# Performance work log

Hardware: AMD Instinct MI355X
Metric: run time of the kernel (lower is better)

## Reference

```python
import jax, jax.numpy as jnp
import numpy as np

DIM, ATT, G, T, KL, B = 1024, 128, 8, 4096, 256, 8
GD = DIM // G
SCALE = 1.0 / np.sqrt(ATT)

def setup_inputs() -> dict:
    key = jax.random.key(0)
    ks = jax.random.split(key, 7)
    x = jax.random.normal(ks[0], (B, T, DIM), dtype=jnp.float32)
    # stacked per-group weights (einsum orientation: in_dim x out_dim)
    Wq = jax.random.normal(ks[1], (G, GD, ATT), dtype=jnp.float32) * (1.0 / np.sqrt(GD))
    Wk = jax.random.normal(ks[2], (G, GD, ATT), dtype=jnp.float32) * (1.0 / np.sqrt(GD))
    Wv = jax.random.normal(ks[3], (G, GD, GD), dtype=jnp.float32) * (1.0 / np.sqrt(GD))
    Wo = jax.random.normal(ks[4], (G, GD, GD), dtype=jnp.float32) * (1.0 / np.sqrt(GD))
    Pk = jax.random.normal(ks[5], (G, T, KL), dtype=jnp.float32) * (1.0 / np.sqrt(T))
    Pv = jax.random.normal(ks[6], (G, T, KL), dtype=jnp.float32) * (1.0 / np.sqrt(T))
    return {"x": x, "Wq": Wq, "Wk": Wk, "Wv": Wv, "Wo": Wo, "Pk": Pk, "Pv": Pv}

def reference(x, Wq, Wk, Wv, Wo, Pk, Pv):
    Bx, Tx, _ = x.shape
    xg = x.reshape(Bx, Tx, G, GD).transpose(0, 2, 1, 3)        # [B,G,T,gd]
    q = jnp.einsum('bgtd,gda->bgta', xg, Wq)                   # [B,G,T,att]
    k = jnp.einsum('bgtd,gda->bgta', xg, Wk)
    v = jnp.einsum('bgtd,gde->bgte', xg, Wv)                   # [B,G,T,gd]
    k_red = jnp.einsum('bgta,gtk->bgka', k, Pk)                # [B,G,kl,att]
    v_red = jnp.einsum('bgte,gtk->bgke', v, Pv)                # [B,G,kl,gd]
    att = jax.nn.softmax(jnp.einsum('bgta,bgka->bgtk', q, k_red) * SCALE, axis=-1)
    out = jnp.einsum('bgtk,bgke->bgte', att, v_red)            # [B,G,T,gd]
    out = jnp.einsum('bgte,gef->bgtf', out, Wo)                # per-group output proj
    return out.transpose(0, 2, 1, 3).reshape(Bx, Tx, DIM)      # concat groups on last dim
```

## Files before the change

### kernel.cpp

```cpp
#include <hip/hip_runtime.h>
#include <hip/hip_bf16.h>

#define NB 8
#define NG 8
#define NT 4096
#define NDIM 1024
#define NGD 128
#define NATT 128
#define NKL 256
#define FSCALE 0.08838834764831845f

typedef __bf16 bf16x8 __attribute__((ext_vector_type(8)));
typedef float f32x4 __attribute__((ext_vector_type(4)));
typedef ushort u16x8 __attribute__((ext_vector_type(8)));
typedef ushort u16x4 __attribute__((ext_vector_type(4)));

#define MFMA(a, b, c) __builtin_amdgcn_mfma_f32_16x16x32_bf16(a, b, c, 0, 0, 0)

__device__ __forceinline__ ushort f2bf(float f) {
  union { float f; unsigned u; } v; v.f = f;
  unsigned r = v.u + 0x7FFFu + ((v.u >> 16) & 1u);
  return (ushort)(r >> 16);
}

__device__ __forceinline__ void gload16(const ushort* g, ushort* l) {
  __builtin_amdgcn_global_load_lds(
      (const __attribute__((address_space(1))) unsigned int*)g,
      (__attribute__((address_space(3))) unsigned int*)l, 16, 0, 0);
}

__global__ __launch_bounds__(512) void k0_weights(
    const float* __restrict__ Wq, const float* __restrict__ Wk,
    const float* __restrict__ Wv, const float* __restrict__ Wo,
    ushort* __restrict__ WkQT, ushort* __restrict__ WvoT) {
  const int sel = blockIdx.x;
  const int g = blockIdx.y;
  __shared__ float A2[128 * 136];
  __shared__ float B2[128 * 136];
  const int tid = threadIdx.x;

  if (sel == 0) {
#pragma unroll
    for (int u = 0; u < 8; ++u) {
      const int c = tid + 512 * u;
      const int row = c >> 5, c4 = (c & 31) * 4;
      *(float4*)&A2[row * 136 + c4] =
          *(const float4*)&Wo[(size_t)g * 16384 + row * 128 + c4];
      const float4 v = *(const float4*)&Wv[(size_t)g * 16384 + row * 128 + c4];
      B2[(c4 + 0) * 136 + row] = v.x;
      B2[(c4 + 1) * 136 + row] = v.y;
      B2[(c4 + 2) * 136 + row] = v.z;
      B2[(c4 + 3) * 136 + row] = v.w;
    }
  } else {
#pragma unroll
    for (int u = 0; u < 8; ++u) {
      const int c = tid + 512 * u;
      const int row = c >> 5, c4 = (c & 31) * 4;
      const float4 q = *(const float4*)&Wq[(size_t)g * 16384 + row * 128 + c4];
      A2[(c4 + 0) * 136 + row] = q.x;
      A2[(c4 + 1) * 136 + row] = q.y;
      A2[(c4 + 2) * 136 + row] = q.z;
      A2[(c4 + 3) * 136 + row] = q.w;
      const float4 k = *(const float4*)&Wk[(size_t)g * 16384 + row * 128 + c4];
      B2[(c4 + 0) * 136 + row] = k.x;
      B2[(c4 + 1) * 136 + row] = k.y;
      B2[(c4 + 2) * 136 + row] = k.z;
      B2[(c4 + 3) * 136 + row] = k.w;
    }
  }
  __syncthreads();

  const int mr = tid >> 4;
  const int mc = tid & 15;
  float acc[4][8];
#pragma unroll
  for (int i = 0; i < 4; ++i)
#pragma unroll
    for (int j = 0; j < 8; ++j) acc[i][j] = 0.f;

#pragma unroll 4
  for (int k = 0; k < 128; ++k) {
    const float4 a = *(const float4*)&A2[k * 136 + mr * 4];
    const float4 b0 = *(const float4*)&B2[k * 136 + mc * 8];
    const float4 b1 = *(const float4*)&B2[k * 136 + mc * 8 + 4];
    const float av[4] = {a.x, a.y, a.z, a.w};
    const float bv[8] = {b0.x, b0.y, b0.z, b0.w, b1.x, b1.y, b1.z, b1.w};
#pragma unroll
    for (int i = 0; i < 4; ++i)
#pragma unroll
      for (int j = 0; j < 8; ++j) acc[i][j] += av[i] * bv[j];
  }

  const float sc = sel ? FSCALE : 1.f;
  ushort* dst = (sel ? WkQT : WvoT) + (size_t)g * 16384;
#pragma unroll
  for (int i = 0; i < 4; ++i) {
    u16x8 pk;
#pragma unroll
    for (int j = 0; j < 8; ++j) pk[j] = f2bf(acc[i][j] * sc);
    *(u16x8*)&dst[(size_t)(mr * 4 + i) * 128 + mc * 8] = pk;
  }
}

__global__ __launch_bounds__(256) void kt_xp(
    const float* __restrict__ x, const float* __restrict__ Pk,
    const float* __restrict__ Pv, ushort* __restrict__ xT,
    ushort* __restrict__ PkT, ushort* __restrict__ PvT) {
  __shared__ float buf[64 * 132];
  const int bid = blockIdx.x;
  const int tid = threadIdx.x;

  if (bid < 4096) {
    const int t0 = (bid & 63) * 64;
    const int bg = bid >> 6;
    const int b = bg >> 3, g = bg & 7;
#pragma unroll
    for (int u = 0; u < 8; ++u) {
      const int c = tid + 256 * u;
      const int row = c >> 5, c4 = (c & 31) * 4;
      *(float4*)&buf[row * 132 + c4] =
          *(const float4*)&x[((size_t)b * NT + t0 + row) * NDIM + g * 128 + c4];
    }
    __syncthreads();
    const int seg = tid & 7;
    const int d0 = tid >> 3;
#pragma unroll
    for (int u = 0; u < 4; ++u) {
      const int d = d0 + u * 32;
      u16x8 pk;
#pragma unroll
      for (int z = 0; z < 8; ++z) pk[z] = f2bf(buf[(seg * 8 + z) * 132 + d]);
      *(u16x8*)&xT[((size_t)bg * 128 + d) * NT + t0 + seg * 8] = pk;
    }
  } else {
    const int idx = bid - 4096;
    const float* P = (idx >> 10) ? Pv : Pk;
    ushort* PT = (idx >> 10) ? PvT : PkT;
    const int r_ = idx & 1023;
    const int t0 = (r_ & 63) * 64;
    const int klh = (r_ >> 6) & 1;
    const int g = (r_ >> 7) & 7;
#pragma unroll
    for (int u = 0; u < 8; ++u) {
      const int c = tid + 256 * u;
      const int row = c >> 5, c4 = (c & 31) * 4;
      *(float4*)&buf[row * 132 + c4] =
          *(const float4*)&P[((size_t)g * NT + t0 + row) * NKL + klh * 128 + c4];
    }
    __syncthreads();
    const int seg = tid & 7;
    const int k0_ = tid >> 3;
#pragma unroll
    for (int u = 0; u < 4; ++u) {
      const int kl = k0_ + u * 32;
      u16x8 pk;
#pragma unroll
      for (int z = 0; z < 8; ++z) pk[z] = f2bf(buf[(seg * 8 + z) * 132 + kl]);
      *(u16x8*)&PT[((size_t)g * NKL + klh * 128 + kl) * NT + t0 + seg * 8] = pk;
    }
  }
}

__global__ __launch_bounds__(256, 2) void k1_mfma(
    const ushort* __restrict__ PkT, const ushort* __restrict__ PvT,
    const ushort* __restrict__ xT, const ushort* __restrict__ WkQT,
    const ushort* __restrict__ WvoT, ushort* __restrict__ MQ,
    ushort* __restrict__ vo_redT) {
  const int bid = blockIdx.x;
  const int work = (bid & 7) * 32 + (bid >> 3);
  const int bg = work >> 2;
  const int sel = (work >> 1) & 1;
  const int klt = work & 1;
  const int g = bg & 7;
  const ushort* PT = (sel ? PvT : PkT) + ((size_t)g * NKL + klt * 128) * NT;
  const ushort* Xb = xT + (size_t)bg * 128 * NT;

  __shared__ ushort lds[32768];

  const int tid = threadIdx.x;
  const int w = tid >> 6, lane = tid & 63;
  const int l15 = lane & 15, l4 = lane >> 4;
  const int rh = (w & 1) * 64;
  const int ch = (w >> 1) * 64;
  const int srow = lane >> 3, sc = lane & 7;

  f32x4 acc[4][4];
  const f32x4 fz = {0.f, 0.f, 0.f, 0.f};
#pragma unroll
  for (int i = 0; i < 4; ++i)
#pragma unroll
    for (int j = 0; j < 4; ++j) acc[i][j] = fz;

#define K1_STAGE(buf, s)                                                      \
  {                                                                           \
    const int t0_ = (s) * 64;                                                 \
    ushort* Ab_ = &lds[(buf) * 16384];                                        \
    ushort* Bb_ = &lds[(buf) * 16384 + 8192];                                 \
    _Pragma("unroll") for (int u = 0; u < 4; ++u) {                           \
      const int row_ = w * 32 + u * 8 + srow;                                 \
      const size_t off_ = (size_t)row_ * NT + t0_ + ((sc ^ (row_ & 7)) << 3); \
      gload16(PT + off_, Ab_ + (w * 32 + u * 8) * 64);                        \
      gload16(Xb + off_, Bb_ + (w * 32 + u * 8) * 64);                        \
    }                                                                         \
  }

#define K1_COMPUTE(buf)                                                       \
  {                                                                           \
    const ushort* Ab_ = &lds[(buf) * 16384];                                  \
    const ushort* Bb_ = &lds[(buf) * 16384 + 8192];                           \
    _Pragma("unroll") for (int h = 0; h < 2; ++h) {                           \
      bf16x8 af_[4], bf_[4];                                                  \
      _Pragma("unroll") for (int i = 0; i < 4; ++i) {                         \
        const int row_ = rh + i * 16 + l15;                                   \
        af_[i] = *(const bf16x8*)&Ab_[row_ * 64 +                             \
                                      (((h * 4 + l4) ^ (row_ & 7)) << 3)];    \
      }                                                                       \
      _Pragma("unroll") for (int j = 0; j < 4; ++j) {                         \
        const int row_ = ch + j * 16 + l15;                                   \
        bf_[j] = *(const bf16x8*)&Bb_[row_ * 64 +                             \
                                      (((h * 4 + l4) ^ (row_ & 7)) << 3)];    \
      }                                                                       \
      _Pragma("unroll") for (int i = 0; i < 4; ++i)                           \
        _Pragma("unroll") for (int j = 0; j < 4; ++j)                         \
          acc[i][j] = MFMA(af_[i], bf_[j], acc[i][j]);                        \
    }                                                                         \
  }

  K1_STAGE(0, 0);
  __syncthreads();
  int buf = 0;
#pragma unroll 1
  for (int s = 0; s < 64; ++s) {
    if (s + 1 < 64) K1_STAGE(buf ^ 1, s + 1);
    K1_COMPUTE(buf);
    __syncthreads();
    buf ^= 1;
  }

  ushort* C = lds;
#pragma unroll
  for (int i = 0; i < 4; ++i)
#pragma unroll
    for (int j = 0; j < 4; ++j)
#pragma unroll
      for (int r = 0; r < 4; ++r)
        C[(rh + i * 16 + l4 * 4 + r) * 136 + ch + j * 16 + l15] =
            f2bf(acc[i][j][r]);
  __syncthreads();

  const ushort* WT = (sel ? WvoT : WkQT) + (size_t)g * 16384;
  f32x4 o[4][4];
#pragma unroll
  for (int i = 0; i < 4; ++i)
#pragma unroll
    for (int j = 0; j < 4; ++j) o[i][j] = fz;
#pragma unroll
  for (int ks = 0; ks < 4; ++ks) {
    bf16x8 af[4], bfr[4];
#pragma unroll
    for (int i = 0; i < 4; ++i)
      af[i] = *(const bf16x8*)&C[(rh + i * 16 + l15) * 136 + ks * 32 + l4 * 8];
#pragma unroll
    for (int j = 0; j < 4; ++j)
      bfr[j] = *(const bf16x8*)&WT[(size_t)(ch + j * 16 + l15) * 128 + ks * 32 + l4 * 8];
#pragma unroll
    for (int i = 0; i < 4; ++i)
#pragma unroll
      for (int j = 0; j < 4; ++j) o[i][j] = MFMA(af[i], bfr[j], o[i][j]);
  }

  if (sel == 0) {
#pragma unroll
    for (int i = 0; i < 4; ++i)
#pragma unroll
      for (int j = 0; j < 4; ++j)
#pragma unroll
        for (int r = 0; r < 4; ++r)
          MQ[((size_t)bg * NKL + klt * 128 + rh + i * 16 + l4 * 4 + r) * 128 +
             ch + j * 16 + l15] = f2bf(o[i][j][r]);
  } else {
#pragma unroll
    for (int i = 0; i < 4; ++i)
#pragma unroll
      for (int j = 0; j < 4; ++j) {
        u16x4 pk;
#pragma unroll
        for (int r = 0; r < 4; ++r) pk[r] = f2bf(o[i][j][r]);
        *(u16x4*)&vo_redT[((size_t)bg * 128 + ch + j * 16 + l15) * NKL +
                          klt * 128 + rh + i * 16 + l4 * 4] = pk;
      }
  }
}

__global__ __launch_bounds__(512, 2) void k2_attn(
    const float* __restrict__ x, const ushort* __restrict__ MQ,
    const ushort* __restrict__ vo_redT, float* __restrict__ out) {
  const int tc = blockIdx.x;
  const int bg = blockIdx.y;
  const int b = bg >> 3, g = bg & 7;

  __shared__ ushort mq[256 * 136];
  __shared__ ushort att[64 * 264];
  __shared__ float redm[2][64];
  __shared__ float reds[2][64];

  const int tid = threadIdx.x;
  const int w = tid >> 6, lane = tid & 63;
  const int l15 = lane & 15, l4 = lane >> 4;
  const int tw = w >> 1, half = w & 1;
  const f32x4 fz = {0.f, 0.f, 0.f, 0.f};

  {
    const ushort* src = MQ + (size_t)bg * NKL * 128;
#pragma unroll
    for (int u = 0; u < 8; ++u) {
      const int c = tid + 512 * u;
      const int r = c >> 4, c8 = (c & 15) * 8;
      *(u16x8*)&mq[r * 136 + c8] = *(const u16x8*)&src[r * 128 + c8];
    }
  }

  const float* xb = x + ((size_t)b * NT + tc * 512) * NDIM + g * 128;
  const ushort* vo = vo_redT + ((size_t)bg * 128 + half * 64) * NKL;

  float4 xr[8];
#pragma unroll
  for (int ks = 0; ks < 4; ++ks) {
    const float* p = xb + (size_t)(tw * 16 + l15) * NDIM + ks * 32 + l4 * 8;
    xr[ks * 2] = *(const float4*)p;
    xr[ks * 2 + 1] = *(const float4*)(p + 4);
  }
  __syncthreads();

#pragma unroll 1
  for (int st = 0; st < 8; ++st) {
    bf16x8 a[4];
#pragma unroll
    for (int ks = 0; ks < 4; ++ks) {
      bf16x8 t;
      t[0] = (__bf16)xr[ks * 2].x; t[1] = (__bf16)xr[ks * 2].y;
      t[2] = (__bf16)xr[ks * 2].z; t[3] = (__bf16)xr[ks * 2].w;
      t[4] = (__bf16)xr[ks * 2 + 1].x; t[5] = (__bf16)xr[ks * 2 + 1].y;
      t[6] = (__bf16)xr[ks * 2 + 1].z; t[7] = (__bf16)xr[ks * 2 + 1].w;
      a[ks] = t;
    }
    if (st + 1 < 8) {
      const float* pn = xb + (size_t)((st + 1) * 64 + tw * 16 + l15) * NDIM;
#pragma unroll
      for (int ks = 0; ks < 4; ++ks) {
        xr[ks * 2] = *(const float4*)(pn + ks * 32 + l4 * 8);
        xr[ks * 2 + 1] = *(const float4*)(pn + ks * 32 + l4 * 8 + 4);
      }
    }
    f32x4 s[8];
#pragma unroll
    for (int n = 0; n < 8; ++n) s[n] = fz;
#pragma unroll
    for (int n = 0; n < 8; ++n) {
      const int row = (half * 8 + n) * 16 + l15;
#pragma unroll
      for (int ks = 0; ks < 4; ++ks) {
        const bf16x8 bv = *(const bf16x8*)&mq[row * 136 + ks * 32 + l4 * 8];
        s[n] = MFMA(a[ks], bv, s[n]);
      }
    }
    const int rowbase = tw * 16 + l4 * 4;
    float inv[4];
    {
      float mx[4];
#pragma unroll
      for (int r = 0; r < 4; ++r) {
        float m = s[0][r];
#pragma unroll
        for (int n = 1; n < 8; ++n) m = fmaxf(m, s[n][r]);
#pragma unroll
        for (int off = 1; off < 16; off <<= 1) m = fmaxf(m, __shfl_xor(m, off, 64));
        mx[r] = m;
      }
      if (l15 == 0) {
#pragma unroll
        for (int r = 0; r < 4; ++r) redm[half][rowbase + r] = mx[r];
      }
      __syncthreads();
      float sm[4];
#pragma unroll
      for (int r = 0; r < 4; ++r) {
        const float mg = fmaxf(mx[r], redm[half ^ 1][rowbase + r]);
        float acc = 0.f;
#pragma unroll
        for (int n = 0; n < 8; ++n) {
          const float p = __expf(s[n][r] - mg);
          acc += p;
          att[(rowbase + r) * 264 + (half * 8 + n) * 16 + l15] = f2bf(p);
        }
#pragma unroll
        for (int off = 1; off < 16; off <<= 1) acc += __shfl_xor(acc, off, 64);
        sm[r] = acc;
      }
      if (l15 == 0) {
#pragma unroll
        for (int r = 0; r < 4; ++r) reds[half][rowbase + r] = sm[r];
      }
      __syncthreads();
#pragma unroll
      for (int r = 0; r < 4; ++r)
        inv[r] = 1.f / (sm[r] + reds[half ^ 1][rowbase + r]);
    }
    f32x4 oa[4];
#pragma unroll
    for (int j = 0; j < 4; ++j) oa[j] = fz;
#pragma unroll
    for (int ks = 0; ks < 8; ++ks) {
      const bf16x8 av = *(const bf16x8*)&att[(tw * 16 + l15) * 264 + ks * 32 + l4 * 8];
#pragma unroll
      for (int j = 0; j < 4; ++j) {
        const bf16x8 bv = *(const bf16x8*)&vo[(size_t)(j * 16 + l15) * NKL + ks * 32 + l4 * 8];
        oa[j] = MFMA(av, bv, oa[j]);
      }
    }
    float* ob = out + ((size_t)b * NT + tc * 512 + st * 64 + tw * 16) * NDIM +
                g * 128 + half * 64;
#pragma unroll
    for (int j = 0; j < 4; ++j)
#pragma unroll
      for (int r = 0; r < 4; ++r)
        ob[(size_t)(l4 * 4 + r) * NDIM + j * 16 + l15] = oa[j][r] * inv[r];
  }
}

extern "C" void kernel_launch(void* const* d_in, const int* in_sizes, int n_in,
                              void* d_out, int out_size, void* d_ws, size_t ws_size,
                              hipStream_t stream) {
  (void)in_sizes; (void)n_in; (void)out_size; (void)ws_size;
  const float* x  = (const float*)d_in[0];
  const float* Wq = (const float*)d_in[1];
  const float* Wk = (const float*)d_in[2];
  const float* Wv = (const float*)d_in[3];
  const float* Wo = (const float*)d_in[4];
  const float* Pk = (const float*)d_in[5];
  const float* Pv = (const float*)d_in[6];

  ushort* wsu = (ushort*)d_ws;
  ushort* PkT     = wsu;
  ushort* PvT     = PkT + 8388608;
  ushort* WkQT    = PvT + 8388608;
  ushort* WvoT    = WkQT + 131072;
  ushort* MQ      = WvoT + 131072;
  ushort* vo_redT = MQ + 2097152;
  ushort* xT = (ushort*)d_out;

  k0_weights<<<dim3(2, NG), dim3(512), 0, stream>>>(Wq, Wk, Wv, Wo, WkQT, WvoT);
  kt_xp<<<dim3(4096 + 2048), dim3(256), 0, stream>>>(x, Pk, Pv, xT, PkT, PvT);
  k1_mfma<<<dim3(256), dim3(256), 0, stream>>>(PkT, PvT, xT, WkQT, WvoT,
                                               MQ, vo_redT);
  k2_attn<<<dim3(8, 64), dim3(512), 0, stream>>>(x, MQ, vo_redT, (float*)d_out);
}
```

Measured before the change: 242.7 us.

## Give each wave full query rows with online softmax, removing block barriers

Result: slower. 464.8 us (+91.5%).

```diff
diff --git a/kernel.cpp b/kernel.cpp
--- a/kernel.cpp
+++ b/kernel.cpp
@@ -301,14 +301,12 @@
   const int b = bg >> 3, g = bg & 7;
 
   __shared__ ushort mq[256 * 136];
-  __shared__ ushort att[64 * 264];
-  __shared__ float redm[2][64];
-  __shared__ float reds[2][64];
+  __shared__ ushort att[8 * 16 * 136];
 
   const int tid = threadIdx.x;
   const int w = tid >> 6, lane = tid & 63;
   const int l15 = lane & 15, l4 = lane >> 4;
-  const int tw = w >> 1, half = w & 1;
+  ushort* attw = att + w * (16 * 136);
   const f32x4 fz = {0.f, 0.f, 0.f, 0.f};
 
   {
@@ -322,53 +320,43 @@
   }
 
   const float* xb = x + ((size_t)b * NT + tc * 512) * NDIM + g * 128;
-  const ushort* vo = vo_redT + ((size_t)bg * 128 + half * 64) * NKL;
-
-  float4 xr[8];
-#pragma unroll
-  for (int ks = 0; ks < 4; ++ks) {
-    const float* p = xb + (size_t)(tw * 16 + l15) * NDIM + ks * 32 + l4 * 8;
-    xr[ks * 2] = *(const float4*)p;
-    xr[ks * 2 + 1] = *(const float4*)(p + 4);
-  }
+  const ushort* vo = vo_redT + (size_t)bg * 128 * NKL;
   __syncthreads();
 
 #pragma unroll 1
-  for (int st = 0; st < 8; ++st) {
+  for (int st = 0; st < 4; ++st) {
+    const float* xrow = xb + (size_t)(st * 128 + w * 16 + l15) * NDIM;
     bf16x8 a[4];
 #pragma unroll
     for (int ks = 0; ks < 4; ++ks) {
+      const float4 u0 = *(const float4*)(xrow + ks * 32 + l4 * 8);
+      const float4 u1 = *(const float4*)(xrow + ks * 32 + l4 * 8 + 4);
       bf16x8 t;
-      t[0] = (__bf16)xr[ks * 2].x; t[1] = (__bf16)xr[ks * 2].y;
-      t[2] = (__bf16)xr[ks * 2].z; t[3] = (__bf16)xr[ks * 2].w;
-      t[4] = (__bf16)xr[ks * 2 + 1].x; t[5] = (__bf16)xr[ks * 2 + 1].y;
-      t[6] = (__bf16)xr[ks * 2 + 1].z; t[7] = (__bf16)xr[ks * 2 + 1].w;
+      t[0] = (__bf16)u0.x; t[1] = (__bf16)u0.y; t[2] = (__bf16)u0.z; t[3] = (__bf16)u0.w;
+      t[4] = (__bf16)u1.x; t[5] = (__bf16)u1.y; t[6] = (__bf16)u1.z; t[7] = (__bf16)u1.w;
       a[ks] = t;
     }
-    if (st + 1 < 8) {
-      const float* pn = xb + (size_t)((st + 1) * 64 + tw * 16 + l15) * NDIM;
-#pragma unroll
-      for (int ks = 0; ks < 4; ++ks) {
-        xr[ks * 2] = *(const float4*)(pn + ks * 32 + l4 * 8);
-        xr[ks * 2 + 1] = *(const float4*)(pn + ks * 32 + l4 * 8 + 4);
-      }
-    }
-    f32x4 s[8];
-#pragma unroll
-    for (int n = 0; n < 8; ++n) s[n] = fz;
-#pragma unroll
-    for (int n = 0; n < 8; ++n) {
-      const int row = (half * 8 + n) * 16 + l15;
-#pragma unroll
-      for (int ks = 0; ks < 4; ++ks) {
-        const bf16x8 bv = *(const bf16x8*)&mq[row * 136 + ks * 32 + l4 * 8];
-        s[n] = MFMA(a[ks], bv, s[n]);
-      }
-    }
-    const int rowbase = tw * 16 + l4 * 4;
-    float inv[4];
-    {
-      float mx[4];
+
+    f32x4 oa[8];
+#pragma unroll
+    for (int dt = 0; dt < 8; ++dt) oa[dt] = fz;
+    float mrun[4], lrun[4];
+
+#pragma unroll
+    for (int h = 0; h < 2; ++h) {
+      f32x4 s[8];
+#pragma unroll
+      for (int n = 0; n < 8; ++n) s[n] = fz;
+#pragma unroll
+      for (int n = 0; n < 8; ++n) {
+        const int row = (h * 8 + n) * 16 + l15;
+#pragma unroll
+        for (int ks = 0; ks < 4; ++ks) {
+          const bf16x8 bv = *(const bf16x8*)&mq[row * 136 + ks * 32 + l4 * 8];
+          s[n] = MFMA(a[ks], bv, s[n]);
+        }
+      }
+      float mh[4];
 #pragma unroll
       for (int r = 0; r < 4; ++r) {
         float m = s[0][r];
@@ -376,56 +364,63 @@
         for (int n = 1; n < 8; ++n) m = fmaxf(m, s[n][r]);
 #pragma unroll
         for (int off = 1; off < 16; off <<= 1) m = fmaxf(m, __shfl_xor(m, off, 64));
-        mx[r] = m;
-      }
-      if (l15 == 0) {
-#pragma unroll
-        for (int r = 0; r < 4; ++r) redm[half][rowbase + r] = mx[r];
-      }
-      __syncthreads();
-      float sm[4];
+        mh[r] = m;
+      }
+      float mnew[4];
+      if (h == 0) {
+#pragma unroll
+        for (int r = 0; r < 4; ++r) { mnew[r] = mh[r]; mrun[r] = mh[r]; lrun[r] = 0.f; }
+      } else {
+#pragma unroll
+        for (int r = 0; r < 4; ++r) {
+          mnew[r] = fmaxf(mrun[r], mh[r]);
+          const float sc = __expf(mrun[r] - mnew[r]);
+          lrun[r] *= sc;
+          mrun[r] = mnew[r];
+#pragma unroll
+          for (int dt = 0; dt < 8; ++dt) oa[dt][r] *= sc;
+        }
+      }
+      f32x4 sum4 = fz;
+#pragma unroll
+      for (int n = 0; n < 8; ++n) {
+#pragma unroll
+        for (int r = 0; r < 4; ++r) {
+          const float p = __expf(s[n][r] - mnew[r]);
+          sum4[r] += p;
+          attw[(l4 * 4 + r) * 136 + n * 16 + l15] = f2bf(p);
+        }
+      }
 #pragma unroll
       for (int r = 0; r < 4; ++r) {
-        const float mg = fmaxf(mx[r], redm[half ^ 1][rowbase + r]);
-        float acc = 0.f;
-#pragma unroll
-        for (int n = 0; n < 8; ++n) {
-          const float p = __expf(s[n][r] - mg);
-          acc += p;
-          att[(rowbase + r) * 264 + (half * 8 + n) * 16 + l15] = f2bf(p);
+        float sh = sum4[r];
+#pragma unroll
+        for (int off = 1; off < 16; off <<= 1) sh += __shfl_xor(sh, off, 64);
+        lrun[r] += sh;
+      }
+      bf16x8 attf[4];
+#pragma unroll
+      for (int ks = 0; ks < 4; ++ks)
+        attf[ks] = *(const bf16x8*)&attw[l15 * 136 + ks * 32 + l4 * 8];
+#pragma unroll
+      for (int ks = 0; ks < 4; ++ks)
+#pragma unroll
+        for (int dt = 0; dt < 8; ++dt) {
+          const bf16x8 vf = *(const bf16x8*)&vo[(size_t)(dt * 16 + l15) * NKL +
+                                                h * 128 + ks * 32 + l4 * 8];
+          oa[dt] = MFMA(attf[ks], vf, oa[dt]);
         }
-#pragma unroll
-        for (int off = 1; off < 16; off <<= 1) acc += __shfl_xor(acc, off, 64);
-        sm[r] = acc;
-      }
-      if (l15 == 0) {
-#pragma unroll
-        for (int r = 0; r < 4; ++r) reds[half][rowbase + r] = sm[r];
-      }
-      __syncthreads();
+    }
+
+    float inv[4];
+#pragma unroll
+    for (int r = 0; r < 4; ++r) inv[r] = 1.f / lrun[r];
+    float* ob = out + ((size_t)b * NT + tc * 512 + st * 128 + w * 16) * NDIM + g * 128;
+#pragma unroll
+    for (int dt = 0; dt < 8; ++dt)
 #pragma unroll
       for (int r = 0; r < 4; ++r)
-        inv[r] = 1.f / (sm[r] + reds[half ^ 1][rowbase + r]);
-    }
-    f32x4 oa[4];
-#pragma unroll
-    for (int j = 0; j < 4; ++j) oa[j] = fz;
-#pragma unroll
-    for (int ks = 0; ks < 8; ++ks) {
-      const bf16x8 av = *(const bf16x8*)&att[(tw * 16 + l15) * 264 + ks * 32 + l4 * 8];
-#pragma unroll
-      for (int j = 0; j < 4; ++j) {
-        const bf16x8 bv = *(const bf16x8*)&vo[(size_t)(j * 16 + l15) * NKL + ks * 32 + l4 * 8];
-        oa[j] = MFMA(av, bv, oa[j]);
-      }
-    }
-    float* ob = out + ((size_t)b * NT + tc * 512 + st * 64 + tw * 16) * NDIM +
-                g * 128 + half * 64;
-#pragma unroll
-    for (int j = 0; j < 4; ++j)
-#pragma unroll
-      for (int r = 0; r < 4; ++r)
-        ob[(size_t)(l4 * 4 + r) * NDIM + j * 16 + l15] = oa[j][r] * inv[r];
+        ob[(size_t)(l4 * 4 + r) * NDIM + dt * 16 + l15] = oa[dt][r] * inv[r];
   }
 }
 
```
